# Kernel optimization log

Measured on AMD Instinct MI355X. Metric: run time of the kernel, lower is better.

Reference implementation:

```python
import jax, jax.numpy as jnp
import numpy as np

# norse LIFParameters defaults with v_th overridden to 0.33
DT = 1e-3
TAU_SYN_INV = 200.0   # 1/5e-3
TAU_MEM_INV = 100.0   # 1/1e-2
V_TH = 0.33
ALPHA = 100.0         # SuperSpike surrogate slope
SEQ_LEN = 32

@jax.custom_vjp
def superspike(x):
    # Heaviside forward, SuperSpike surrogate backward (norse method='super')
    return (x > 0).astype(x.dtype)

def _ss_fwd(x):
    return superspike(x), x

def _ss_bwd(x, g):
    return (g / (ALPHA * jnp.abs(x) + 1.0) ** 2,)

superspike.defvjp(_ss_fwd, _ss_bwd)

def _encode(current):
    # ConstantCurrentLIFEncoder: LIF current encoder, constant input current
    def step(v, _):
        v = v + DT * TAU_MEM_INV * (-v + current)
        z = superspike(v - V_TH)
        v = v - z * v  # v_reset = 0
        return v, z
    _, spikes = jax.lax.scan(step, jnp.zeros_like(current), None, length=SEQ_LEN)
    return spikes  # [T, B, F]

def _lif_step(inp, v, i):
    # norse lif_feed_forward_step (v_leak=0, v_reset=0)
    v_dec = v + DT * TAU_MEM_INV * (-v + i)
    i_dec = i * (1.0 - DT * TAU_SYN_INV)
    z = superspike(v_dec - V_TH)
    return z, v_dec * (1.0 - z), i_dec + inp

def setup_inputs() -> dict:
    key = jax.random.key(0)
    ks = jax.random.split(key, 6)
    B, F_IN, N_CLASSES = 2048, 2048, 100  # F_IN = 2*input_size
    def lin_w(k, out_f, in_f):
        bound = 1.0 / np.sqrt(in_f)
        return jax.random.uniform(k, (out_f, in_f), jnp.float32, -bound, bound)
    return {
        "x": jax.random.normal(ks[0], (B, F_IN), jnp.float32),
        "w1": lin_w(ks[1], 512, F_IN),
        "w2": lin_w(ks[2], 512, 512),
        "w3": lin_w(ks[3], 256, 512),
        "w_out": lin_w(ks[4], N_CLASSES, 256),
        "feature_scalar": jnp.ones((1,), jnp.float32),
        "encoder_scalar": jnp.ones((1,), jnp.float32),
    }

def reference(x, w1, w2, w3, w_out, feature_scalar, encoder_scalar):
    B = x.shape[0]
    n_classes = w_out.shape[0]
    # encoder + scaling (dropout is identity in eval mode)
    spikes = 5.0 * encoder_scalar * _encode(2.0 * feature_scalar * x)  # [T,B,F]

    def step(carry, z_t):
        v1, i1, v2, i2, v3, i3, vo, io = carry
        s1, v1, i1 = _lif_step(z_t @ w1.T, v1, i1)
        s2, v2, i2 = _lif_step(s1 @ w2.T, v2, i2)
        s3, v3, i3 = _lif_step(s2 @ w3.T, v3, i3)
        # LILinearCell (leaky integrator, no spike)
        vo = vo + DT * TAU_MEM_INV * (-vo + io)
        io = io * (1.0 - DT * TAU_SYN_INV) + s3 @ w_out.T
        return (v1, i1, v2, i2, v3, i3, vo, io), None

    z = lambda *s: jnp.zeros(s, x.dtype)
    init = (z(B, 512), z(B, 512), z(B, 512), z(B, 512),
            z(B, 256), z(B, 256), z(B, n_classes), z(B, n_classes))
    final, _ = jax.lax.scan(step, init, spikes)
    # decode = voltages[-1] == LI membrane voltage at last timestep
    return final[6]
```

## Files before the change

kernel.cpp:

```cpp
#include <hip/hip_runtime.h>
#include <cstddef>


#define THREADS 256

#define WOFF1 0
#define WOFF2 1048576
#define WOFF3 1310720
#define WOFF4 1441792
#define WTOT  1474560

__global__ __launch_bounds__(THREADS) void prep_kernel(
    const float* __restrict__ w1, const float* __restrict__ w2,
    const float* __restrict__ w3, const float* __restrict__ w4,
    float* __restrict__ wt)
{
  int idx = blockIdx.x * THREADS + threadIdx.x;
  if (idx >= WTOT) return;
  if (idx < WOFF2) {
    int j = idx >> 9, o = idx & 511;
    wt[idx] = w1[o * 2048 + j];
  } else if (idx < WOFF3) {
    int r = idx - WOFF2, j = r >> 9, o = r & 511;
    wt[idx] = w2[o * 512 + j];
  } else if (idx < WOFF4) {
    int r = idx - WOFF3, j = r >> 8, o = r & 255;
    wt[idx] = w3[o * 512 + j];
  } else {
    int r = idx - WOFF4, j = r >> 7, o = r & 127;
    wt[idx] = (o < 100) ? w4[o * 256 + j] : 0.0f;
  }
}

__global__ __launch_bounds__(THREADS) void enc_kernel(
    const float* __restrict__ x, const float* __restrict__ fscale,
    unsigned* __restrict__ em, int b0)
{
  int idx = blockIdx.x * THREADS + threadIdx.x;
  int b = idx >> 11, j = idx & 2047;
  float c = 2.0f * fscale[0] * x[((size_t)(b0 + b) << 11) + j];
  float v = 0.0f;
  unsigned m = 0u;
#pragma unroll
  for (int t = 0; t < 32; ++t) {
    v = v + 0.1f * (c - v);
    unsigned z = ((v - 0.33f) > 0.0f) ? 1u : 0u;
    m |= z << t;
    if (z) v = 0.0f;
  }
  em[idx] = m;
}

template <int O, bool FINAL>
__global__ __launch_bounds__(THREADS, 2) void gemm_sparse(
    const unsigned* __restrict__ mIn, const float* __restrict__ WT,
    int J, const float* __restrict__ es,
    unsigned* __restrict__ mOut, float* __restrict__ out, int bbase)
{
  constexpr int NAO = (O >= 256) ? 4 : 2;
  constexpr int WPB = O / (64 * NAO);
  constexpr int BPB = 4 / WPB;
  typedef float fv __attribute__((ext_vector_type(NAO)));
  const int tid = threadIdx.x;
  const int lane = tid & 63, wvid = tid >> 6;
  const int b = blockIdx.x * BPB + wvid / WPB;
  const int obase = (wvid % WPB) * (64 * NAO) + lane * NAO;
  const float* const wbase = WT + obase;
  float scalef = es ? 5.0f * es[0] : 1.0f;
  const int scale_i =
      __builtin_amdgcn_readfirstlane(__float_as_int(scalef));

  float acc[32][NAO];
#pragma unroll
  for (int t = 0; t < 32; ++t)
#pragma unroll
    for (int k = 0; k < NAO; ++k) acc[t][k] = 0.0f;

  const unsigned* mrow = mIn + (size_t)b * J;
  const int NW = J >> 6;

  auto wloadU = [&](int g, fv* wv) {
#pragma unroll
    for (int jj = 0; jj < 4; ++jj)
      wv[jj] = *(const fv*)(wbase + (size_t)(g * 4 + jj) * O);
  };
  auto fma_group = [&](unsigned mw, int q, const fv* wv) {
#pragma unroll
    for (int jj = 0; jj < 4; ++jj) {
      unsigned w = (unsigned)__builtin_amdgcn_readlane((int)mw, q * 4 + jj);
      if (w) {
#pragma unroll
        for (int t = 0; t < 32; ++t) {
          float av = (w & (1u << t)) ? __int_as_float(scale_i) : 0.0f;
#pragma unroll
          for (int k = 0; k < NAO; ++k)
            acc[t][k] = fmaf(av, wv[jj][k], acc[t][k]);
        }
      }
    }
  };

  fv wvA[4], wvB[4], wvC[4], wvD[4];
  unsigned mwC = mrow[lane];
  wloadU(0, wvA);
  wloadU(1, wvB);
#pragma unroll 1
  for (int w = 0; w < NW; ++w) {
    unsigned mwN = mrow[((w + 1 < NW) ? (w + 1) << 6 : w << 6) + lane];
    const int gb = w << 4;
#pragma unroll 1
    for (int q = 0; q < 16; q += 4) {
      const int g = gb + q;
      wloadU(g + 2, wvC);
      fma_group(mwC, q + 0, wvA);
      wloadU(g + 3, wvD);
      fma_group(mwC, q + 1, wvB);
      wloadU(g + 4, wvA);
      fma_group(mwC, q + 2, wvC);
      wloadU(g + 5, wvB);
      fma_group(mwC, q + 3, wvD);
    }
    mwC = mwN;
  }

#pragma unroll
  for (int k = 0; k < NAO; ++k) {
    if (FINAL) {
      float v = 0.0f, cur = 0.0f;
#pragma unroll
      for (int t2 = 0; t2 < 32; ++t2) {
        v = v + 0.1f * (cur - v);
        cur = 0.8f * cur + acc[t2][k];
      }
      int o = obase + k;
      if (o < 100) out[(size_t)(bbase + b) * 100 + o] = v;
    } else {
      float v = 0.0f, cur = 0.0f;
      unsigned zw = 0u;
#pragma unroll
      for (int t2 = 0; t2 < 32; ++t2) {
        v = v + 0.1f * (cur - v);
        unsigned z = ((v - 0.33f) > 0.0f) ? 1u : 0u;
        zw |= z << t2;
        if (z) v = 0.0f;
        cur = 0.8f * cur + acc[t2][k];
      }
      mOut[(size_t)b * O + obase + k] = zw;
    }
  }
}

extern "C" void kernel_launch(void* const* d_in, const int* in_sizes, int n_in,
                              void* d_out, int out_size, void* d_ws, size_t ws_size,
                              hipStream_t stream)
{
  const float* x  = (const float*)d_in[0];
  const float* w1 = (const float*)d_in[1];
  const float* w2 = (const float*)d_in[2];
  const float* w3 = (const float*)d_in[3];
  const float* w4 = (const float*)d_in[4];
  const float* fs = (const float*)d_in[5];
  const float* es = (const float*)d_in[6];
  float* out = (float*)d_out;
  (void)in_sizes; (void)n_in; (void)out_size;

  int Bc = 2048;
  auto need = [](int bc) -> size_t {
    return ((size_t)WTOT + (size_t)bc * (2048 + 512 + 512 + 256)) * 4;
  };
  while (Bc > 64 && need(Bc) > ws_size) Bc >>= 1;

  float* WT = (float*)d_ws;
  unsigned* em  = (unsigned*)(WT + WTOT);
  unsigned* s1m = em  + (size_t)Bc * 2048;
  unsigned* s2m = s1m + (size_t)Bc * 512;
  unsigned* s3m = s2m + (size_t)Bc * 512;

  prep_kernel<<<(WTOT + THREADS - 1) / THREADS, THREADS, 0, stream>>>(
      w1, w2, w3, w4, WT);

  for (int b0 = 0; b0 < 2048; b0 += Bc) {
    enc_kernel<<<(Bc * 2048) / THREADS, THREADS, 0, stream>>>(x, fs, em, b0);
    gemm_sparse<512, false><<<Bc / 2, THREADS, 0, stream>>>(
        em, WT + WOFF1, 2048, es, s1m, nullptr, 0);
    gemm_sparse<512, false><<<Bc / 2, THREADS, 0, stream>>>(
        s1m, WT + WOFF2, 512, nullptr, s2m, nullptr, 0);
    gemm_sparse<256, false><<<Bc / 4, THREADS, 0, stream>>>(
        s2m, WT + WOFF3, 512, nullptr, s3m, nullptr, 0);
    gemm_sparse<128, true><<<Bc / 4, THREADS, 0, stream>>>(
        s3m, WT + WOFF4, 256, nullptr, nullptr, out, b0);
  }
}
```

Baseline: 1.327 ms.

## Split spike GEMM across time halves per wave with LDS handoff of LIF state

Each wave now covers all output neurons of a batch row for one 16-timestep half, instead of half the outputs over all 32 timesteps. Input words are skipped per 16-bit half, so time halves with no spikes skip their FMAs. The LIF recurrence is chained across the halves: the first wave writes its voltage, current and spike bits to LDS, a barrier follows, and the second wave continues. This adds duplicated weight loads per wave and a serialized epilogue across two waves. It also changes the launch grid for the smaller layers.

```diff
diff --git a/kernel.cpp b/kernel.cpp
--- a/kernel.cpp
+++ b/kernel.cpp
@@ -57,41 +57,47 @@
     int J, const float* __restrict__ es,
     unsigned* __restrict__ mOut, float* __restrict__ out, int bbase)
 {
-  constexpr int NAO = (O >= 256) ? 4 : 2;
-  constexpr int WPB = O / (64 * NAO);
-  constexpr int BPB = 4 / WPB;
+  constexpr int NAO = O / 64;
   typedef float fv __attribute__((ext_vector_type(NAO)));
   const int tid = threadIdx.x;
   const int lane = tid & 63, wvid = tid >> 6;
-  const int b = blockIdx.x * BPB + wvid / WPB;
-  const int obase = (wvid % WPB) * (64 * NAO) + lane * NAO;
-  const float* const wbase = WT + obase;
+  const int bl = wvid >> 1;
+  const int th = wvid & 1;
+  const int b = blockIdx.x * 2 + bl;
+  const int ob = lane * NAO;
+  const float* const wbase = WT + ob;
+  const unsigned tsh = (unsigned)(th << 4);
   float scalef = es ? 5.0f * es[0] : 1.0f;
   const int scale_i =
       __builtin_amdgcn_readfirstlane(__float_as_int(scalef));
 
-  float acc[32][NAO];
-#pragma unroll
-  for (int t = 0; t < 32; ++t)
+  __shared__ float    ls_v[2][O];
+  __shared__ float    ls_c[2][O];
+  __shared__ unsigned ls_z[2][O];
+
+  float acc[16][NAO];
+#pragma unroll
+  for (int t = 0; t < 16; ++t)
 #pragma unroll
     for (int k = 0; k < NAO; ++k) acc[t][k] = 0.0f;
 
   const unsigned* mrow = mIn + (size_t)b * J;
   const int NW = J >> 6;
 
-  auto wloadU = [&](int g, fv* wv) {
-#pragma unroll
-    for (int jj = 0; jj < 4; ++jj)
-      wv[jj] = *(const fv*)(wbase + (size_t)(g * 4 + jj) * O);
+  auto wload = [&](int g, fv* wv) {
+#pragma unroll
+    for (int r = 0; r < 2; ++r)
+      wv[r] = *(const fv*)(wbase + (size_t)(g * 2 + r) * O);
   };
-  auto fma_group = [&](unsigned mw, int q, const fv* wv) {
-#pragma unroll
-    for (int jj = 0; jj < 4; ++jj) {
-      unsigned w = (unsigned)__builtin_amdgcn_readlane((int)mw, q * 4 + jj);
-      if (w) {
-#pragma unroll
-        for (int t = 0; t < 32; ++t) {
-          float av = (w & (1u << t)) ? __int_as_float(scale_i) : 0.0f;
+  auto fg = [&](unsigned mw, int q2, const fv* wv) {
+#pragma unroll
+    for (int jj = 0; jj < 2; ++jj) {
+      unsigned w = (unsigned)__builtin_amdgcn_readlane((int)mw, q2 * 2 + jj);
+      unsigned wh = (w >> tsh) & 0xFFFFu;
+      if (wh) {
+#pragma unroll
+        for (int t = 0; t < 16; ++t) {
+          float av = __int_as_float((int)((wh >> t) & 1u) * scale_i);
 #pragma unroll
           for (int k = 0; k < NAO; ++k)
             acc[t][k] = fmaf(av, wv[jj][k], acc[t][k]);
@@ -100,52 +106,71 @@
     }
   };
 
-  fv wvA[4], wvB[4], wvC[4], wvD[4];
+  fv wvA[2], wvB[2], wvC[2], wvD[2];
   unsigned mwC = mrow[lane];
-  wloadU(0, wvA);
-  wloadU(1, wvB);
+  wload(0, wvA);
+  wload(1, wvB);
 #pragma unroll 1
   for (int w = 0; w < NW; ++w) {
     unsigned mwN = mrow[((w + 1 < NW) ? (w + 1) << 6 : w << 6) + lane];
-    const int gb = w << 4;
+    const int gb = w << 5;
 #pragma unroll 1
-    for (int q = 0; q < 16; q += 4) {
+    for (int q = 0; q < 32; q += 4) {
       const int g = gb + q;
-      wloadU(g + 2, wvC);
-      fma_group(mwC, q + 0, wvA);
-      wloadU(g + 3, wvD);
-      fma_group(mwC, q + 1, wvB);
-      wloadU(g + 4, wvA);
-      fma_group(mwC, q + 2, wvC);
-      wloadU(g + 5, wvB);
-      fma_group(mwC, q + 3, wvD);
+      wload(g + 2, wvC);
+      fg(mwC, q + 0, wvA);
+      wload(g + 3, wvD);
+      fg(mwC, q + 1, wvB);
+      wload(g + 4, wvA);
+      fg(mwC, q + 2, wvC);
+      wload(g + 5, wvB);
+      fg(mwC, q + 3, wvD);
     }
     mwC = mwN;
   }
 
-#pragma unroll
-  for (int k = 0; k < NAO; ++k) {
-    if (FINAL) {
-      float v = 0.0f, cur = 0.0f;
-#pragma unroll
-      for (int t2 = 0; t2 < 32; ++t2) {
-        v = v + 0.1f * (cur - v);
-        cur = 0.8f * cur + acc[t2][k];
-      }
-      int o = obase + k;
-      if (o < 100) out[(size_t)(bbase + b) * 100 + o] = v;
-    } else {
+  if (th == 0) {
+#pragma unroll
+    for (int k = 0; k < NAO; ++k) {
       float v = 0.0f, cur = 0.0f;
       unsigned zw = 0u;
 #pragma unroll
-      for (int t2 = 0; t2 < 32; ++t2) {
+      for (int t2 = 0; t2 < 16; ++t2) {
         v = v + 0.1f * (cur - v);
-        unsigned z = ((v - 0.33f) > 0.0f) ? 1u : 0u;
-        zw |= z << t2;
-        if (z) v = 0.0f;
+        if (!FINAL) {
+          unsigned z = ((v - 0.33f) > 0.0f) ? 1u : 0u;
+          zw |= z << t2;
+          if (z) v = 0.0f;
+        }
         cur = 0.8f * cur + acc[t2][k];
       }
-      mOut[(size_t)b * O + obase + k] = zw;
+      ls_v[bl][ob + k] = v;
+      ls_c[bl][ob + k] = cur;
+      if (!FINAL) ls_z[bl][ob + k] = zw;
+    }
+  }
+  __syncthreads();
+  if (th == 1) {
+#pragma unroll
+    for (int k = 0; k < NAO; ++k) {
+      float v = ls_v[bl][ob + k], cur = ls_c[bl][ob + k];
+      unsigned zw = FINAL ? 0u : ls_z[bl][ob + k];
+#pragma unroll
+      for (int t2 = 0; t2 < 16; ++t2) {
+        v = v + 0.1f * (cur - v);
+        if (!FINAL) {
+          unsigned z = ((v - 0.33f) > 0.0f) ? 1u : 0u;
+          zw |= z << (16 + t2);
+          if (z) v = 0.0f;
+        }
+        cur = 0.8f * cur + acc[t2][k];
+      }
+      if (FINAL) {
+        int o = ob + k;
+        if (o < 100) out[(size_t)(bbase + b) * 100 + o] = v;
+      } else {
+        mOut[(size_t)b * O + ob + k] = zw;
+      }
     }
   }
 }
@@ -185,9 +210,9 @@
         em, WT + WOFF1, 2048, es, s1m, nullptr, 0);
     gemm_sparse<512, false><<<Bc / 2, THREADS, 0, stream>>>(
         s1m, WT + WOFF2, 512, nullptr, s2m, nullptr, 0);
-    gemm_sparse<256, false><<<Bc / 4, THREADS, 0, stream>>>(
+    gemm_sparse<256, false><<<Bc / 2, THREADS, 0, stream>>>(
         s2m, WT + WOFF3, 512, nullptr, s3m, nullptr, 0);
-    gemm_sparse<128, true><<<Bc / 4, THREADS, 0, stream>>>(
+    gemm_sparse<128, true><<<Bc / 2, THREADS, 0, stream>>>(
         s3m, WT + WOFF4, 256, nullptr, nullptr, out, b0);
   }
 }
```

New measurement: 1.449 ms. +9.2%, slower.

## Give each wave a full output row and restructure sparse spike-GEMM pipeline

Applied to the files above, without the earlier changes.

Each wave now covers all O outputs of one batch row (NAO = O/64), so one spike-mask readlane drives more FMAs and blocks hold four rows. The weight prefetch pipeline drops from four to two buffers, and readlane extraction of mask words is hoisted ahead of the FMA groups. The per-timestep select becomes a branchless shift-and-mask. For O=512 this means 256 accumulators per thread, so launch bounds drop to 1 block per CU, trading occupancy and spill risk for fewer redundant mask scans.

```diff
diff --git a/kernel.cpp b/kernel.cpp
--- a/kernel.cpp
+++ b/kernel.cpp
@@ -52,20 +52,18 @@
 }
 
 template <int O, bool FINAL>
-__global__ __launch_bounds__(THREADS, 2) void gemm_sparse(
+__global__ __launch_bounds__(THREADS, 1) void gemm_sparse(
     const unsigned* __restrict__ mIn, const float* __restrict__ WT,
     int J, const float* __restrict__ es,
     unsigned* __restrict__ mOut, float* __restrict__ out, int bbase)
 {
-  constexpr int NAO = (O >= 256) ? 4 : 2;
-  constexpr int WPB = O / (64 * NAO);
-  constexpr int BPB = 4 / WPB;
+  constexpr int NAO = O / 64;
   typedef float fv __attribute__((ext_vector_type(NAO)));
   const int tid = threadIdx.x;
   const int lane = tid & 63, wvid = tid >> 6;
-  const int b = blockIdx.x * BPB + wvid / WPB;
-  const int obase = (wvid % WPB) * (64 * NAO) + lane * NAO;
-  const float* const wbase = WT + obase;
+  const int b = blockIdx.x * 4 + wvid;
+  const int ob = lane * NAO;
+  const float* const wbase = WT + ob;
   float scalef = es ? 5.0f * es[0] : 1.0f;
   const int scale_i =
       __builtin_amdgcn_readfirstlane(__float_as_int(scalef));
@@ -84,14 +82,19 @@
     for (int jj = 0; jj < 4; ++jj)
       wv[jj] = *(const fv*)(wbase + (size_t)(g * 4 + jj) * O);
   };
-  auto fma_group = [&](unsigned mw, int q, const fv* wv) {
+  auto rl4 = [&](unsigned mw, int grp, unsigned* w) {
+#pragma unroll
+    for (int jj = 0; jj < 4; ++jj)
+      w[jj] = (unsigned)__builtin_amdgcn_readlane((int)mw, grp * 4 + jj);
+  };
+  auto fma_group = [&](const unsigned* w, const fv* wv) {
 #pragma unroll
     for (int jj = 0; jj < 4; ++jj) {
-      unsigned w = (unsigned)__builtin_amdgcn_readlane((int)mw, q * 4 + jj);
-      if (w) {
+      if (w[jj]) {
 #pragma unroll
         for (int t = 0; t < 32; ++t) {
-          float av = (w & (1u << t)) ? __int_as_float(scale_i) : 0.0f;
+          float av = __int_as_float(
+              (int)((((int)(w[jj] << (31 - t))) >> 31) & scale_i));
 #pragma unroll
           for (int k = 0; k < NAO; ++k)
             acc[t][k] = fmaf(av, wv[jj][k], acc[t][k]);
@@ -100,25 +103,25 @@
     }
   };
 
-  fv wvA[4], wvB[4], wvC[4], wvD[4];
+  unsigned wA[4], wB[4];
+  fv wvA[4], wvB[4];
   unsigned mwC = mrow[lane];
+  rl4(mwC, 0, wA);
   wloadU(0, wvA);
-  wloadU(1, wvB);
 #pragma unroll 1
   for (int w = 0; w < NW; ++w) {
     unsigned mwN = mrow[((w + 1 < NW) ? (w + 1) << 6 : w << 6) + lane];
     const int gb = w << 4;
 #pragma unroll 1
-    for (int q = 0; q < 16; q += 4) {
+    for (int q = 0; q < 16; q += 2) {
       const int g = gb + q;
-      wloadU(g + 2, wvC);
-      fma_group(mwC, q + 0, wvA);
-      wloadU(g + 3, wvD);
-      fma_group(mwC, q + 1, wvB);
-      wloadU(g + 4, wvA);
-      fma_group(mwC, q + 2, wvC);
-      wloadU(g + 5, wvB);
-      fma_group(mwC, q + 3, wvD);
+      rl4(mwC, q + 1, wB);
+      wloadU(g + 1, wvB);
+      fma_group(wA, wvA);
+      wloadU(g + 2, wvA);
+      fma_group(wB, wvB);
+      unsigned msrc = (q + 2 < 16) ? mwC : mwN;
+      rl4(msrc, (q + 2) & 15, wA);
     }
     mwC = mwN;
   }
@@ -132,7 +135,7 @@
         v = v + 0.1f * (cur - v);
         cur = 0.8f * cur + acc[t2][k];
       }
-      int o = obase + k;
+      int o = ob + k;
       if (o < 100) out[(size_t)(bbase + b) * 100 + o] = v;
     } else {
       float v = 0.0f, cur = 0.0f;
@@ -145,7 +148,7 @@
         if (z) v = 0.0f;
         cur = 0.8f * cur + acc[t2][k];
       }
-      mOut[(size_t)b * O + obase + k] = zw;
+      mOut[(size_t)b * O + ob + k] = zw;
     }
   }
 }
@@ -181,9 +184,9 @@
 
   for (int b0 = 0; b0 < 2048; b0 += Bc) {
     enc_kernel<<<(Bc * 2048) / THREADS, THREADS, 0, stream>>>(x, fs, em, b0);
-    gemm_sparse<512, false><<<Bc / 2, THREADS, 0, stream>>>(
+    gemm_sparse<512, false><<<Bc / 4, THREADS, 0, stream>>>(
         em, WT + WOFF1, 2048, es, s1m, nullptr, 0);
-    gemm_sparse<512, false><<<Bc / 2, THREADS, 0, stream>>>(
+    gemm_sparse<512, false><<<Bc / 4, THREADS, 0, stream>>>(
         s1m, WT + WOFF2, 512, nullptr, s2m, nullptr, 0);
     gemm_sparse<256, false><<<Bc / 4, THREADS, 0, stream>>>(
         s2m, WT + WOFF3, 512, nullptr, s3m, nullptr, 0);
```

New measurement: 1.466 ms. 10.4% more time.

## Skip inactive inputs via ballot and split time across lanes in sparse GEMM

Applied to the files above, without the earlier changes.

Restructures the spike-mask GEMM so each wave covers 64 outputs, with lanes split into 16 time slots times 4 output groups, each lane holding 2 time steps across 16 outputs. Inputs whose 32-step spike mask is all zero are skipped with a ballot and ctz loop instead of being tested one by one, and the per-output time recurrence runs after a transpose through shared memory. This cuts accumulator registers from 128 to 32 per lane, allows 4 blocks per CU, and quadruples the grid. In exchange, each active input now costs four 16-byte weight loads per lane instead of register-pipelined prefetches, and the kernel needs shared memory and a block barrier.

```diff
diff --git a/kernel.cpp b/kernel.cpp
--- a/kernel.cpp
+++ b/kernel.cpp
@@ -52,100 +52,99 @@
 }
 
 template <int O, bool FINAL>
-__global__ __launch_bounds__(THREADS, 2) void gemm_sparse(
+__global__ __launch_bounds__(THREADS, 4) void gemm_sparse(
     const unsigned* __restrict__ mIn, const float* __restrict__ WT,
     int J, const float* __restrict__ es,
     unsigned* __restrict__ mOut, float* __restrict__ out, int bbase)
 {
-  constexpr int NAO = (O >= 256) ? 4 : 2;
-  constexpr int WPB = O / (64 * NAO);
-  constexpr int BPB = 4 / WPB;
-  typedef float fv __attribute__((ext_vector_type(NAO)));
+  typedef float fv4 __attribute__((ext_vector_type(4)));
+  constexpr int WPB = O / 64;
   const int tid = threadIdx.x;
   const int lane = tid & 63, wvid = tid >> 6;
-  const int b = blockIdx.x * BPB + wvid / WPB;
-  const int obase = (wvid % WPB) * (64 * NAO) + lane * NAO;
+  const int t16 = lane & 15;
+  const int og  = lane >> 4;
+  int b, obase;
+  if constexpr (WPB >= 4) {
+    constexpr int BLKS = WPB / 4;
+    b = blockIdx.x / BLKS;
+    obase = (blockIdx.x % BLKS) * 256 + wvid * 64;
+  } else {
+    constexpr int BPB = 4 / WPB;
+    b = blockIdx.x * BPB + wvid / WPB;
+    obase = (wvid % WPB) * 64;
+  }
   const float* const wbase = WT + obase;
   float scalef = es ? 5.0f * es[0] : 1.0f;
   const int scale_i =
       __builtin_amdgcn_readfirstlane(__float_as_int(scalef));
 
-  float acc[32][NAO];
+  __shared__ float xp[4][64][34];
+
+  float a0[16], a1[16];
 #pragma unroll
-  for (int t = 0; t < 32; ++t)
-#pragma unroll
-    for (int k = 0; k < NAO; ++k) acc[t][k] = 0.0f;
+  for (int k = 0; k < 16; ++k) { a0[k] = 0.0f; a1[k] = 0.0f; }
 
   const unsigned* mrow = mIn + (size_t)b * J;
   const int NW = J >> 6;
 
-  auto wloadU = [&](int g, fv* wv) {
+  unsigned mwA = mrow[lane];
+#pragma unroll 1
+  for (int w = 0; w < NW; ++w) {
+    unsigned mwB = mrow[((w + 1 < NW) ? (w + 1) : w) * 64 + lane];
+    unsigned long long act = __ballot(mwA != 0u);
+    const float* const wwin = wbase + (size_t)(w << 6) * O;
+    while (act) {
+      int jj = __builtin_ctzll(act);
+      act &= act - 1;
+      unsigned ws = (unsigned)__builtin_amdgcn_readlane((int)mwA, jj);
+      const float* p = wwin + (size_t)jj * O + og * 16;
+      fv4 f0 = *(const fv4*)(p);
+      fv4 f1 = *(const fv4*)(p + 4);
+      fv4 f2 = *(const fv4*)(p + 8);
+      fv4 f3 = *(const fv4*)(p + 12);
+      unsigned sh = ws >> t16;
+      float av0 = __int_as_float((int)(sh & 1u) * scale_i);
+      float av1 = __int_as_float((int)((sh >> 16) & 1u) * scale_i);
 #pragma unroll
-    for (int jj = 0; jj < 4; ++jj)
-      wv[jj] = *(const fv*)(wbase + (size_t)(g * 4 + jj) * O);
-  };
-  auto fma_group = [&](unsigned mw, int q, const fv* wv) {
-#pragma unroll
-    for (int jj = 0; jj < 4; ++jj) {
-      unsigned w = (unsigned)__builtin_amdgcn_readlane((int)mw, q * 4 + jj);
-      if (w) {
-#pragma unroll
-        for (int t = 0; t < 32; ++t) {
-          float av = (w & (1u << t)) ? __int_as_float(scale_i) : 0.0f;
-#pragma unroll
-          for (int k = 0; k < NAO; ++k)
-            acc[t][k] = fmaf(av, wv[jj][k], acc[t][k]);
-        }
+      for (int c = 0; c < 4; ++c) {
+        a0[c]      = fmaf(av0, f0[c], a0[c]);
+        a1[c]      = fmaf(av1, f0[c], a1[c]);
+        a0[4 + c]  = fmaf(av0, f1[c], a0[4 + c]);
+        a1[4 + c]  = fmaf(av1, f1[c], a1[4 + c]);
+        a0[8 + c]  = fmaf(av0, f2[c], a0[8 + c]);
+        a1[8 + c]  = fmaf(av1, f2[c], a1[8 + c]);
+        a0[12 + c] = fmaf(av0, f3[c], a0[12 + c]);
+        a1[12 + c] = fmaf(av1, f3[c], a1[12 + c]);
       }
     }
-  };
-
-  fv wvA[4], wvB[4], wvC[4], wvD[4];
-  unsigned mwC = mrow[lane];
-  wloadU(0, wvA);
-  wloadU(1, wvB);
-#pragma unroll 1
-  for (int w = 0; w < NW; ++w) {
-    unsigned mwN = mrow[((w + 1 < NW) ? (w + 1) << 6 : w << 6) + lane];
-    const int gb = w << 4;
-#pragma unroll 1
-    for (int q = 0; q < 16; q += 4) {
-      const int g = gb + q;
-      wloadU(g + 2, wvC);
-      fma_group(mwC, q + 0, wvA);
-      wloadU(g + 3, wvD);
-      fma_group(mwC, q + 1, wvB);
-      wloadU(g + 4, wvA);
-      fma_group(mwC, q + 2, wvC);
-      wloadU(g + 5, wvB);
-      fma_group(mwC, q + 3, wvD);
-    }
-    mwC = mwN;
+    mwA = mwB;
   }
 
 #pragma unroll
-  for (int k = 0; k < NAO; ++k) {
-    if (FINAL) {
-      float v = 0.0f, cur = 0.0f;
+  for (int k = 0; k < 16; ++k) {
+    xp[wvid][og * 16 + k][t16]      = a0[k];
+    xp[wvid][og * 16 + k][t16 + 16] = a1[k];
+  }
+  __syncthreads();
+  {
+    float v = 0.0f, cur = 0.0f;
+    unsigned zw = 0u;
 #pragma unroll
-      for (int t2 = 0; t2 < 32; ++t2) {
-        v = v + 0.1f * (cur - v);
-        cur = 0.8f * cur + acc[t2][k];
-      }
-      int o = obase + k;
-      if (o < 100) out[(size_t)(bbase + b) * 100 + o] = v;
-    } else {
-      float v = 0.0f, cur = 0.0f;
-      unsigned zw = 0u;
-#pragma unroll
-      for (int t2 = 0; t2 < 32; ++t2) {
-        v = v + 0.1f * (cur - v);
+    for (int t2 = 0; t2 < 32; ++t2) {
+      float a = xp[wvid][lane][t2];
+      v = v + 0.1f * (cur - v);
+      if (!FINAL) {
         unsigned z = ((v - 0.33f) > 0.0f) ? 1u : 0u;
         zw |= z << t2;
         if (z) v = 0.0f;
-        cur = 0.8f * cur + acc[t2][k];
       }
-      mOut[(size_t)b * O + obase + k] = zw;
+      cur = 0.8f * cur + a;
+    }
+    if (FINAL) {
+      int o = obase + lane;
+      if (o < 100) out[(size_t)(bbase + b) * 100 + o] = v;
+    } else {
+      mOut[(size_t)b * O + obase + lane] = zw;
     }
   }
 }
@@ -181,13 +180,13 @@
 
   for (int b0 = 0; b0 < 2048; b0 += Bc) {
     enc_kernel<<<(Bc * 2048) / THREADS, THREADS, 0, stream>>>(x, fs, em, b0);
-    gemm_sparse<512, false><<<Bc / 2, THREADS, 0, stream>>>(
+    gemm_sparse<512, false><<<Bc * 2, THREADS, 0, stream>>>(
         em, WT + WOFF1, 2048, es, s1m, nullptr, 0);
-    gemm_sparse<512, false><<<Bc / 2, THREADS, 0, stream>>>(
+    gemm_sparse<512, false><<<Bc * 2, THREADS, 0, stream>>>(
         s1m, WT + WOFF2, 512, nullptr, s2m, nullptr, 0);
-    gemm_sparse<256, false><<<Bc / 4, THREADS, 0, stream>>>(
+    gemm_sparse<256, false><<<Bc, THREADS, 0, stream>>>(
         s2m, WT + WOFF3, 512, nullptr, s3m, nullptr, 0);
-    gemm_sparse<128, true><<<Bc / 4, THREADS, 0, stream>>>(
+    gemm_sparse<128, true><<<Bc / 2, THREADS, 0, stream>>>(
         s3m, WT + WOFF4, 256, nullptr, nullptr, out, b0);
   }
 }
```

New measurement: 2.373 ms. 1.79x slower.
